# Kernel tuning notes

Measured on AMD Instinct MI355X. Metric: run time of the kernel, lower is better.

The kernel has to match this reference:

```python
import jax, jax.numpy as jnp
import numpy as np

B, T, C = 4, 1024, 1024
H, L = 16, 256
D = C // H  # head_dim = 64


def setup_inputs() -> dict:
    key = jax.random.key(0)
    ks = jax.random.split(key, 10)
    s = lambda fan_in: 1.0 / np.sqrt(fan_in)
    return {
        "x": jax.random.normal(ks[0], (B, T, C), jnp.float32),
        "padding_mask": jax.random.randint(ks[1], (B, T), 0, 2, jnp.int32),
        "interaction_matrix": jax.random.normal(ks[2], (B, T, T, H), jnp.float32),
        # weights stored [in, out] (x @ W == torch Linear with W = weight.T)
        "W_ckv": jax.random.uniform(ks[3], (C, L), jnp.float32, -s(C), s(C)),
        "W_cq": jax.random.uniform(ks[4], (C, L), jnp.float32, -s(C), s(C)),
        "W_kc": jax.random.uniform(ks[5], (L, C), jnp.float32, -s(L), s(L)),
        "W_qc": jax.random.uniform(ks[6], (L, C), jnp.float32, -s(L), s(L)),
        "W_vc": jax.random.uniform(ks[7], (L, C), jnp.float32, -s(L), s(L)),
        "W_proj": jax.random.uniform(ks[8], (C, C), jnp.float32, -s(C), s(C)),
        "b_proj": jax.random.uniform(ks[9], (C,), jnp.float32, -s(C), s(C)),
    }


def reference(x, padding_mask, interaction_matrix, W_ckv, W_cq, W_kc, W_qc, W_vc, W_proj, b_proj):
    # low-rank down/up projections
    kv_down = x @ W_ckv                      # [B,T,L]
    q_down = x @ W_cq                        # [B,T,L]
    k = (kv_down @ W_kc).reshape(B, T, H, D).transpose(0, 2, 1, 3)  # [B,H,T,D]
    q = (q_down @ W_qc).reshape(B, T, H, D).transpose(0, 2, 1, 3)
    v = (kv_down @ W_vc).reshape(B, T, H, D).transpose(0, 2, 1, 3)

    scores = jnp.einsum("bhqd,bhkd->bhqk", q, k) * (D ** -0.5)      # [B,H,T,T]

    # padding mask (fix=False path): mask[b,t]==0 masks query row t, fill -1e9
    row_mask = padding_mask[:, None, :, None]                        # [B,1,T,1]
    scores = jnp.where(row_mask == 0, jnp.float32(-1e9), scores)

    # causal mask
    causal = jnp.tril(jnp.ones((T, T), jnp.bool_))
    scores = jnp.where(causal, scores, -jnp.inf)

    # additive interaction bias: [B,T,T,H].transpose(1,3) -> [B,H,T,T]
    scores = scores + interaction_matrix.transpose(0, 3, 2, 1)

    attn = jax.nn.softmax(scores, axis=-1)                           # dropout=0 (eval)
    ctx = jnp.einsum("bhqk,bhkd->bhqd", attn, v)                     # [B,H,T,D]
    ctx = ctx.transpose(0, 2, 1, 3).reshape(B, T, C)
    return ctx @ W_proj + b_proj
```

## Files before the change

### kernel.cpp

```cpp
#include <hip/hip_runtime.h>

typedef unsigned short u16;
typedef unsigned int u32;
typedef __attribute__((ext_vector_type(8))) __bf16 bf16x8;
typedef __attribute__((ext_vector_type(4))) float f32x4;
typedef __attribute__((ext_vector_type(4))) short s16x4;
typedef __attribute__((ext_vector_type(4))) u32 u32x4;

#define LOG2E 1.4426950408889634f
#define NINF (-__builtin_inff())

static constexpr size_t OFF_WT_CKV = 0;
static constexpr size_t OFF_WT_CQ  = 262144;
static constexpr size_t OFF_WT_KC  = 524288;
static constexpr size_t OFF_WT_QC  = 786432;
static constexpr size_t OFF_WT_VC  = 1048576;
static constexpr size_t OFF_WT_PROJ= 1310720;
static constexpr size_t OFF_XBF    = 2359296;
static constexpr size_t OFF_DQ     = OFF_XBF + 4194304;
static constexpr size_t OFF_KB     = OFF_DQ  + 2097152;
static constexpr size_t OFF_QB     = OFF_KB  + 4194304;
static constexpr size_t OFF_VTB    = OFF_QB  + 4194304;
static constexpr size_t OFF_CTX    = OFF_XBF;

__device__ __forceinline__ u16 f2bf(float f) {
  u32 u = __builtin_bit_cast(u32, f);
  u = (u + 0x7fffu + ((u >> 16) & 1u)) >> 16;
  return (u16)u;
}

__device__ __forceinline__ void gld16(const void* g, void* l) {
  __builtin_amdgcn_global_load_lds(
      (const __attribute__((address_space(1))) u32*)(unsigned long long)g,
      (__attribute__((address_space(3))) u32*)(u32)(unsigned long long)l,
      16, 0, 0);
}

__global__ __launch_bounds__(256) void convert_kernel(
    const float* __restrict__ xin, const float* __restrict__ w0,
    const float* __restrict__ w1, const float* __restrict__ w2,
    const float* __restrict__ w3, const float* __restrict__ w4,
    const float* __restrict__ w5, u16* __restrict__ ws) {
  int gid = blockIdx.x * 256 + threadIdx.x;
  if (gid < 524288) {
    int i0 = gid * 8;
    f32x4 a = *(const f32x4*)(xin + i0);
    f32x4 b = *(const f32x4*)(xin + i0 + 4);
    u32x4 pv;
    pv[0] = (u32)f2bf(a[0]) | ((u32)f2bf(a[1]) << 16);
    pv[1] = (u32)f2bf(a[2]) | ((u32)f2bf(a[3]) << 16);
    pv[2] = (u32)f2bf(b[0]) | ((u32)f2bf(b[1]) << 16);
    pv[3] = (u32)f2bf(b[2]) | ((u32)f2bf(b[3]) << 16);
    *(u32x4*)(ws + OFF_XBF + i0) = pv;
    return;
  }
  int id = gid - 524288;
  if (id < 262144) { int k = id >> 8, n = id & 255;
    ws[OFF_WT_CKV + (size_t)n*1024 + k] = f2bf(w0[id]); return; }
  id -= 262144;
  if (id < 262144) { int k = id >> 8, n = id & 255;
    ws[OFF_WT_CQ + (size_t)n*1024 + k] = f2bf(w1[id]); return; }
  id -= 262144;
  if (id < 262144) { int k = id >> 10, n = id & 1023;
    ws[OFF_WT_KC + (size_t)n*256 + k] = f2bf(w2[id]); return; }
  id -= 262144;
  if (id < 262144) { int k = id >> 10, n = id & 1023;
    ws[OFF_WT_QC + (size_t)n*256 + k] = f2bf(w3[id]); return; }
  id -= 262144;
  if (id < 262144) { int k = id >> 10, n = id & 1023;
    ws[OFF_WT_VC + (size_t)n*256 + k] = f2bf(w4[id]); return; }
  id -= 262144;
  if (id < 1048576) { int k = id >> 10, n = id & 1023;
    ws[OFF_WT_PROJ + (size_t)n*1024 + k] = f2bf(w5[id]); return; }
}

template<int MODE, int MT, int NT>
__global__ __launch_bounds__(256, (MT == 128) ? 2 : 4) void gemm_kernel(
    const u16* __restrict__ A, const u16* __restrict__ BT,
    u16* __restrict__ ws, float* __restrict__ out, const float* __restrict__ bias) {
  constexpr int KDIM = (MODE == 1) ? 256 : 1024;
  constexpr int LDA  = (MODE == 1) ? 512 : 1024;
  constexpr int MW = MT / 32;
  constexpr int NW = NT / 32;
  __shared__ u16 lA[MT*32];
  __shared__ u16 lB[NT*32];
  const int t = threadIdx.x;
  const int lane = t & 63;
  const int c = lane & 15, quad = lane >> 4;
  const int w = t >> 6, wr = w >> 1, wc = w & 1;
  const int gm0 = blockIdx.y * MT, ct0 = blockIdx.x * NT;
  const u16* Ae = A;
  int out_id = 0;
  if (MODE == 1) { out_id = ct0 >> 10; if (out_id == 1) Ae += 256; }
  const int m0s = t >> 2, q0s = t & 3;

  f32x4 acc[MW][NW];
  #pragma unroll
  for (int i = 0; i < MW; ++i)
    #pragma unroll
    for (int j = 0; j < NW; ++j) acc[i][j] = (f32x4)0.0f;

  for (int k0 = 0; k0 < KDIM; k0 += 32) {
    __syncthreads();
    gld16(Ae + (size_t)(gm0 + m0s)*LDA + k0 + q0s*8, (char*)lA + t*16);
    if (MT == 128)
      gld16(Ae + (size_t)(gm0 + m0s + 64)*LDA + k0 + q0s*8, (char*)lA + (t+256)*16);
    gld16(BT + (size_t)(ct0 + m0s)*KDIM + k0 + q0s*8, (char*)lB + t*16);
    if (NT == 128)
      gld16(BT + (size_t)(ct0 + m0s + 64)*KDIM + k0 + q0s*8, (char*)lB + (t+256)*16);
    __syncthreads();
    bf16x8 af[MW], bfr[NW];
    #pragma unroll
    for (int mt = 0; mt < MW; ++mt)
      af[mt] = *(const bf16x8*)(lA + (wr*(MT/2) + mt*16 + c)*32 + quad*8);
    #pragma unroll
    for (int nt = 0; nt < NW; ++nt)
      bfr[nt] = *(const bf16x8*)(lB + (wc*(NT/2) + nt*16 + c)*32 + quad*8);
    #pragma unroll
    for (int mt = 0; mt < MW; ++mt)
      #pragma unroll
      for (int nt = 0; nt < NW; ++nt)
        acc[mt][nt] = __builtin_amdgcn_mfma_f32_16x16x32_bf16(af[mt], bfr[nt], acc[mt][nt], 0, 0, 0);
  }

  const int rbase = gm0 + wr*(MT/2);
  const int cbase = ct0 + wc*(NT/2);
  if (MODE == 0) {
    #pragma unroll
    for (int mt = 0; mt < MW; ++mt)
      #pragma unroll
      for (int nt = 0; nt < NW; ++nt)
        #pragma unroll
        for (int j = 0; j < 4; ++j) {
          int row = rbase + mt*16 + quad*4 + j;
          int col = cbase + nt*16 + c;
          ws[OFF_DQ + (size_t)row*512 + col] = f2bf(acc[mt][nt][j]);
        }
  } else if (MODE == 2) {
    float bv[NW];
    #pragma unroll
    for (int nt = 0; nt < NW; ++nt) bv[nt] = bias[cbase + nt*16 + c];
    #pragma unroll
    for (int mt = 0; mt < MW; ++mt)
      #pragma unroll
      for (int nt = 0; nt < NW; ++nt)
        #pragma unroll
        for (int j = 0; j < 4; ++j) {
          int row = rbase + mt*16 + quad*4 + j;
          out[(size_t)row*1024 + cbase + nt*16 + c] = acc[mt][nt][j] + bv[nt];
        }
  } else {
    const int cl = (ct0 & 1023) + wc*64;
    const int hcol = cl >> 6;
    if (out_id == 2) {
      #pragma unroll
      for (int mt = 0; mt < MW; ++mt) {
        int row0 = rbase + mt*16 + quad*4;
        int bb = row0 >> 10, t0 = row0 & 1023;
        #pragma unroll
        for (int nt = 0; nt < NW; ++nt) {
          int d = nt*16 + c;
          s16x4 pk;
          #pragma unroll
          for (int j = 0; j < 4; ++j) pk[j] = (short)f2bf(acc[mt][nt][j]);
          *(s16x4*)(ws + OFF_VTB + (((size_t)bb*16 + hcol)*64 + d)*1024 + t0) = pk;
        }
      }
    } else {
      const float sc = out_id ? 0.125f : 1.0f;
      const size_t base = out_id ? OFF_QB : OFF_KB;
      #pragma unroll
      for (int mt = 0; mt < MW; ++mt)
        #pragma unroll
        for (int nt = 0; nt < NW; ++nt)
          #pragma unroll
          for (int j = 0; j < 4; ++j) {
            int row = rbase + mt*16 + quad*4 + j;
            int bb = row >> 10, tt = row & 1023;
            ws[base + ((((size_t)bb*16 + hcol)*1024 + tt)<<6) + nt*16 + c]
                = f2bf(acc[mt][nt][j]*sc);
          }
    }
  }
}

__global__ __launch_bounds__(512, 2) void attn_kernel(
    const u16* __restrict__ Kb, const u16* __restrict__ Qb,
    const u16* __restrict__ VTb, u16* __restrict__ ctx,
    const float* __restrict__ im, const int* __restrict__ pmask) {
  __shared__ float lim[32*196];
  __shared__ u16   lp[8][16*40];

  const int t = threadIdx.x, lane = t & 63, w = t >> 6;
  const int c = lane & 15, quad = lane >> 4;
  const int bi = blockIdx.x;
  const int g = bi >> 4, hh = (bi >> 3) & 1, s = bi & 7;
  const int b = s >> 1, pair = g*2 + (s & 1);
  const int h0 = hh*8, h = h0 + w;
  const size_t bh = ((size_t)b*16 + h) << 16;

  const int k0s = t >> 5, q0s = (t & 31) >> 1, hp0 = (t & 1) * 4;
  const float* imb = im + ((size_t)b << 24) + h0;
  float* l0 = lim + k0s*196 + q0s*12 + hp0;
  float* l1 = lim + (k0s + 16)*196 + q0s*12 + hp0;

  const int qtA = 63 - pair;
  f32x4 r0 = *(const f32x4*)(imb + (((size_t)k0s)*1024 + qtA*16 + q0s)*16 + hp0);
  f32x4 r1 = *(const f32x4*)(imb + (((size_t)(k0s+16))*1024 + qtA*16 + q0s)*16 + hp0);

  for (int pass = 0; pass < 2; ++pass) {
    const int qt = pass ? pair : qtA;
    const int qrow0 = qt * 16;
    const int ktmax = (qrow0 + 15) >> 5;

    bf16x8 qf0 = *(const bf16x8*)(Qb + bh + (size_t)(qrow0 + c)*64 + quad*8);
    bf16x8 qf1 = *(const bf16x8*)(Qb + bh + (size_t)(qrow0 + c)*64 + 32 + quad*8);

    int tq[4], rm[4];
    #pragma unroll
    for (int j = 0; j < 4; ++j) {
      tq[j] = qrow0 + quad*4 + j;
      rm[j] = pmask[b*1024 + tq[j]];
    }
    float mr[4] = {NINF, NINF, NINF, NINF};
    float lr[4] = {0.f, 0.f, 0.f, 0.f};
    f32x4 O[4] = {(f32x4)0.f, (f32x4)0.f, (f32x4)0.f, (f32x4)0.f};

    for (int kt = 0; kt <= ktmax; ++kt) {
      const int kb = kt*32;
      __syncthreads();
      *(f32x4*)l0 = r0;
      *(f32x4*)l1 = r1;
      __syncthreads();
      if (kt < ktmax) {
        r0 = *(const f32x4*)(imb + (((size_t)(kb + 32 + k0s))*1024 + qrow0 + q0s)*16 + hp0);
        r1 = *(const f32x4*)(imb + (((size_t)(kb + 48 + k0s))*1024 + qrow0 + q0s)*16 + hp0);
      } else if (pass == 0) {
        r0 = *(const f32x4*)(imb + (((size_t)k0s)*1024 + pair*16 + q0s)*16 + hp0);
        r1 = *(const f32x4*)(imb + (((size_t)(k0s+16))*1024 + pair*16 + q0s)*16 + hp0);
      }

      f32x4 S[2] = {(f32x4)0.f, (f32x4)0.f};
      #pragma unroll
      for (int nt = 0; nt < 2; ++nt) {
        const u16* kp = Kb + bh + (size_t)(kb + nt*16 + c)*64 + quad*8;
        bf16x8 kf0 = *(const bf16x8*)kp;
        bf16x8 kf1 = *(const bf16x8*)(kp + 32);
        S[nt] = __builtin_amdgcn_mfma_f32_16x16x32_bf16(qf0, kf0, S[nt], 0, 0, 0);
        S[nt] = __builtin_amdgcn_mfma_f32_16x16x32_bf16(qf1, kf1, S[nt], 0, 0, 0);
      }
      #pragma unroll
      for (int nt = 0; nt < 2; ++nt) {
        int tk = kb + nt*16 + c;
        #pragma unroll
        for (int j = 0; j < 4; ++j) {
          float sv = S[nt][j] + lim[(nt*16 + c)*196 + (quad*4 + j)*12 + w];
          sv = rm[j] ? sv : 0.0f;
          sv = (tk <= tq[j]) ? sv : NINF;
          S[nt][j] = sv;
        }
      }
      float mn[4], al[4];
      #pragma unroll
      for (int j = 0; j < 4; ++j) {
        float vm = fmaxf(S[0][j], S[1][j]);
        vm = fmaxf(vm, __shfl_xor(vm, 1, 64));
        vm = fmaxf(vm, __shfl_xor(vm, 2, 64));
        vm = fmaxf(vm, __shfl_xor(vm, 4, 64));
        vm = fmaxf(vm, __shfl_xor(vm, 8, 64));
        mn[j] = fmaxf(mr[j], vm);
        al[j] = exp2f((mr[j] - mn[j]) * LOG2E);
        mr[j] = mn[j];
      }
      #pragma unroll
      for (int nt = 0; nt < 2; ++nt)
        #pragma unroll
        for (int j = 0; j < 4; ++j)
          S[nt][j] = exp2f((S[nt][j] - mn[j]) * LOG2E);
      #pragma unroll
      for (int j = 0; j < 4; ++j) {
        float sum = S[0][j] + S[1][j];
        sum += __shfl_xor(sum, 1, 64);
        sum += __shfl_xor(sum, 2, 64);
        sum += __shfl_xor(sum, 4, 64);
        sum += __shfl_xor(sum, 8, 64);
        lr[j] = lr[j]*al[j] + sum;
      }
      #pragma unroll
      for (int nd = 0; nd < 4; ++nd)
        #pragma unroll
        for (int j = 0; j < 4; ++j) O[nd][j] *= al[j];
      #pragma unroll
      for (int nt = 0; nt < 2; ++nt)
        #pragma unroll
        for (int j = 0; j < 4; ++j)
          lp[w][(quad*4 + j)*40 + nt*16 + c] = f2bf(S[nt][j]);
      bf16x8 pf = *(const bf16x8*)&lp[w][c*40 + quad*8];
      #pragma unroll
      for (int nd = 0; nd < 4; ++nd) {
        bf16x8 vf = *(const bf16x8*)(VTb + bh + (size_t)(nd*16 + c)*1024 + kb + quad*8);
        O[nd] = __builtin_amdgcn_mfma_f32_16x16x32_bf16(pf, vf, O[nd], 0, 0, 0);
      }
    }

    float inv[4];
    #pragma unroll
    for (int j = 0; j < 4; ++j) inv[j] = 1.0f / lr[j];
    #pragma unroll
    for (int nd = 0; nd < 4; ++nd)
      #pragma unroll
      for (int j = 0; j < 4; ++j)
        ctx[((size_t)b*1024 + tq[j])*1024 + h*64 + nd*16 + c] = f2bf(O[nd][j] * inv[j]);
  }
}

extern "C" void kernel_launch(void* const* d_in, const int* in_sizes, int n_in,
                              void* d_out, int out_size, void* d_ws, size_t ws_size,
                              hipStream_t stream) {
  const float* x     = (const float*)d_in[0];
  const int*   pm    = (const int*)d_in[1];
  const float* im    = (const float*)d_in[2];
  const float* wckv  = (const float*)d_in[3];
  const float* wcq   = (const float*)d_in[4];
  const float* wkc   = (const float*)d_in[5];
  const float* wqc   = (const float*)d_in[6];
  const float* wvc   = (const float*)d_in[7];
  const float* wproj = (const float*)d_in[8];
  const float* bproj = (const float*)d_in[9];
  u16* ws = (u16*)d_ws;
  float* out = (float*)d_out;

  convert_kernel<<<11264, 256, 0, stream>>>(x, wckv, wcq, wkc, wqc, wvc, wproj, ws);
  gemm_kernel<0,64,64><<<dim3(8, 64), 256, 0, stream>>>(ws + OFF_XBF, ws + OFF_WT_CKV, ws, nullptr, nullptr);
  gemm_kernel<1,128,128><<<dim3(24, 32), 256, 0, stream>>>(ws + OFF_DQ, ws + OFF_WT_KC, ws, nullptr, nullptr);
  attn_kernel<<<256, 512, 0, stream>>>(ws + OFF_KB, ws + OFF_QB, ws + OFF_VTB,
                                       ws + OFF_CTX, im, pm);
  gemm_kernel<2,64,128><<<dim3(8, 64), 256, 0, stream>>>(ws + OFF_CTX, ws + OFF_WT_PROJ, ws, out, bproj);
}
```

Baseline: 477.2 us.

## Software-pipeline attention loop with double-buffered bias and register K/V prefetch

Result: faster. 458.9 us (-3.8%).

```diff
diff --git a/kernel.cpp b/kernel.cpp
--- a/kernel.cpp
+++ b/kernel.cpp
@@ -34,6 +34,18 @@
       (const __attribute__((address_space(1))) u32*)(unsigned long long)g,
       (__attribute__((address_space(3))) u32*)(u32)(unsigned long long)l,
       16, 0, 0);
+}
+
+__device__ __forceinline__ void twrite(const float* __restrict__ w, u16* __restrict__ dst,
+                                       int n, int k0, int N, int R) {
+  u32x4 pv;
+  #pragma unroll
+  for (int jj = 0; jj < 4; ++jj) {
+    u32 lo = f2bf(w[(size_t)(k0 + 2*jj) * N + n]);
+    u32 hi = f2bf(w[(size_t)(k0 + 2*jj + 1) * N + n]);
+    pv[jj] = lo | (hi << 16);
+  }
+  *(u32x4*)(dst + (size_t)n * R + k0) = pv;
 }
 
 __global__ __launch_bounds__(256) void convert_kernel(
@@ -55,23 +67,23 @@
     return;
   }
   int id = gid - 524288;
-  if (id < 262144) { int k = id >> 8, n = id & 255;
-    ws[OFF_WT_CKV + (size_t)n*1024 + k] = f2bf(w0[id]); return; }
-  id -= 262144;
-  if (id < 262144) { int k = id >> 8, n = id & 255;
-    ws[OFF_WT_CQ + (size_t)n*1024 + k] = f2bf(w1[id]); return; }
-  id -= 262144;
-  if (id < 262144) { int k = id >> 10, n = id & 1023;
-    ws[OFF_WT_KC + (size_t)n*256 + k] = f2bf(w2[id]); return; }
-  id -= 262144;
-  if (id < 262144) { int k = id >> 10, n = id & 1023;
-    ws[OFF_WT_QC + (size_t)n*256 + k] = f2bf(w3[id]); return; }
-  id -= 262144;
-  if (id < 262144) { int k = id >> 10, n = id & 1023;
-    ws[OFF_WT_VC + (size_t)n*256 + k] = f2bf(w4[id]); return; }
-  id -= 262144;
-  if (id < 1048576) { int k = id >> 10, n = id & 1023;
-    ws[OFF_WT_PROJ + (size_t)n*1024 + k] = f2bf(w5[id]); return; }
+  if (id < 32768)  { int n = id >> 7, k0 = (id & 127) * 8;
+    twrite(w0, ws + OFF_WT_CKV, n, k0, 256, 1024); return; }
+  id -= 32768;
+  if (id < 32768)  { int n = id >> 7, k0 = (id & 127) * 8;
+    twrite(w1, ws + OFF_WT_CQ, n, k0, 256, 1024); return; }
+  id -= 32768;
+  if (id < 32768)  { int n = id >> 5, k0 = (id & 31) * 8;
+    twrite(w2, ws + OFF_WT_KC, n, k0, 1024, 256); return; }
+  id -= 32768;
+  if (id < 32768)  { int n = id >> 5, k0 = (id & 31) * 8;
+    twrite(w3, ws + OFF_WT_QC, n, k0, 1024, 256); return; }
+  id -= 32768;
+  if (id < 32768)  { int n = id >> 5, k0 = (id & 31) * 8;
+    twrite(w4, ws + OFF_WT_VC, n, k0, 1024, 256); return; }
+  id -= 32768;
+  if (id < 131072) { int n = id >> 7, k0 = (id & 127) * 8;
+    twrite(w5, ws + OFF_WT_PROJ, n, k0, 1024, 1024); return; }
 }
 
 template<int MODE, int MT, int NT>
@@ -188,7 +200,7 @@
     const u16* __restrict__ Kb, const u16* __restrict__ Qb,
     const u16* __restrict__ VTb, u16* __restrict__ ctx,
     const float* __restrict__ im, const int* __restrict__ pmask) {
-  __shared__ float lim[32*196];
+  __shared__ float lim[2][32*196];
   __shared__ u16   lp[8][16*40];
 
   const int t = threadIdx.x, lane = t & 63, w = t >> 6;
@@ -196,122 +208,163 @@
   const int bi = blockIdx.x;
   const int g = bi >> 4, hh = (bi >> 3) & 1, s = bi & 7;
   const int b = s >> 1, pair = g*2 + (s & 1);
-  const int h0 = hh*8, h = h0 + w;
+  const int h = hh*8 + w;
   const size_t bh = ((size_t)b*16 + h) << 16;
+  const int qtA = 63 - pair, qtB = pair;
+  const int ntA = ((qtA*16 + 15) >> 5) + 1;
 
   const int k0s = t >> 5, q0s = (t & 31) >> 1, hp0 = (t & 1) * 4;
-  const float* imb = im + ((size_t)b << 24) + h0;
-  float* l0 = lim + k0s*196 + q0s*12 + hp0;
-  float* l1 = lim + (k0s + 16)*196 + q0s*12 + hp0;
-
-  const int qtA = 63 - pair;
-  f32x4 r0 = *(const f32x4*)(imb + (((size_t)k0s)*1024 + qtA*16 + q0s)*16 + hp0);
-  f32x4 r1 = *(const f32x4*)(imb + (((size_t)(k0s+16))*1024 + qtA*16 + q0s)*16 + hp0);
-
-  for (int pass = 0; pass < 2; ++pass) {
-    const int qt = pass ? pair : qtA;
-    const int qrow0 = qt * 16;
-    const int ktmax = (qrow0 + 15) >> 5;
-
-    bf16x8 qf0 = *(const bf16x8*)(Qb + bh + (size_t)(qrow0 + c)*64 + quad*8);
-    bf16x8 qf1 = *(const bf16x8*)(Qb + bh + (size_t)(qrow0 + c)*64 + 32 + quad*8);
-
-    int tq[4], rm[4];
+  const float* imb = im + ((size_t)b << 24) + hh*8;
+  const int loff0 = k0s*196 + q0s*12 + hp0;
+  const int loff1 = (k0s + 16)*196 + q0s*12 + hp0;
+
+  int qrow = qtA * 16;
+  bf16x8 qf0 = *(const bf16x8*)(Qb + bh + (size_t)(qrow + c)*64 + quad*8);
+  bf16x8 qf1 = *(const bf16x8*)(Qb + bh + (size_t)(qrow + c)*64 + 32 + quad*8);
+  int tq[4], rm[4];
+  #pragma unroll
+  for (int j = 0; j < 4; ++j) {
+    tq[j] = qrow + quad*4 + j;
+    rm[j] = pmask[b*1024 + tq[j]];
+  }
+  float mr[4] = {NINF, NINF, NINF, NINF};
+  float lr[4] = {0.f, 0.f, 0.f, 0.f};
+  f32x4 O[4] = {(f32x4)0.f, (f32x4)0.f, (f32x4)0.f, (f32x4)0.f};
+
+  f32x4 r0 = *(const f32x4*)(imb + ((size_t)k0s*1024 + qrow + q0s)*16 + hp0);
+  f32x4 r1 = *(const f32x4*)(imb + ((size_t)(k0s+16)*1024 + qrow + q0s)*16 + hp0);
+  bf16x8 kc00 = *(const bf16x8*)(Kb + bh + (size_t)(c)*64 + quad*8);
+  bf16x8 kc01 = *(const bf16x8*)(Kb + bh + (size_t)(c)*64 + 32 + quad*8);
+  bf16x8 kc10 = *(const bf16x8*)(Kb + bh + (size_t)(16 + c)*64 + quad*8);
+  bf16x8 kc11 = *(const bf16x8*)(Kb + bh + (size_t)(16 + c)*64 + 32 + quad*8);
+  bf16x8 vc[4];
+  #pragma unroll
+  for (int nd = 0; nd < 4; ++nd)
+    vc[nd] = *(const bf16x8*)(VTb + bh + (size_t)(nd*16 + c)*1024 + quad*8);
+  *(f32x4*)(&lim[0][loff0]) = r0;
+  *(f32x4*)(&lim[0][loff1]) = r1;
+  __syncthreads();
+
+  for (int i = 0; i < 33; ++i) {
+    const int cb = i & 1;
+    const int kb = (i < ntA ? i : i - ntA) * 32;
+    const int ip = i + 1;
+    const bool havep = ip < 33;
+
+    bf16x8 kn00, kn01, kn10, kn11, vn[4];
+    if (havep) {
+      const int kbp = (ip < ntA ? ip : ip - ntA) * 32;
+      const int qrp = (ip < ntA ? qtA : qtB) * 16;
+      r0 = *(const f32x4*)(imb + ((size_t)(kbp + k0s)*1024 + qrp + q0s)*16 + hp0);
+      r1 = *(const f32x4*)(imb + ((size_t)(kbp + 16 + k0s)*1024 + qrp + q0s)*16 + hp0);
+      const u16* kp = Kb + bh + (size_t)(kbp + c)*64 + quad*8;
+      kn00 = *(const bf16x8*)kp;
+      kn01 = *(const bf16x8*)(kp + 32);
+      kn10 = *(const bf16x8*)(kp + 1024);
+      kn11 = *(const bf16x8*)(kp + 1056);
+      #pragma unroll
+      for (int nd = 0; nd < 4; ++nd)
+        vn[nd] = *(const bf16x8*)(VTb + bh + (size_t)(nd*16 + c)*1024 + kbp + quad*8);
+    }
+
+    f32x4 S[2] = {(f32x4)0.f, (f32x4)0.f};
+    S[0] = __builtin_amdgcn_mfma_f32_16x16x32_bf16(qf0, kc00, S[0], 0, 0, 0);
+    S[0] = __builtin_amdgcn_mfma_f32_16x16x32_bf16(qf1, kc01, S[0], 0, 0, 0);
+    S[1] = __builtin_amdgcn_mfma_f32_16x16x32_bf16(qf0, kc10, S[1], 0, 0, 0);
+    S[1] = __builtin_amdgcn_mfma_f32_16x16x32_bf16(qf1, kc11, S[1], 0, 0, 0);
+
+    #pragma unroll
+    for (int nt = 0; nt < 2; ++nt) {
+      int tk = kb + nt*16 + c;
+      #pragma unroll
+      for (int j = 0; j < 4; ++j) {
+        float sv = S[nt][j] + lim[cb][(nt*16 + c)*196 + (quad*4 + j)*12 + w];
+        sv = rm[j] ? sv : 0.0f;
+        sv = (tk <= tq[j]) ? sv : NINF;
+        S[nt][j] = sv;
+      }
+    }
+    float mn[4], al[4];
     #pragma unroll
     for (int j = 0; j < 4; ++j) {
-      tq[j] = qrow0 + quad*4 + j;
-      rm[j] = pmask[b*1024 + tq[j]];
-    }
-    float mr[4] = {NINF, NINF, NINF, NINF};
-    float lr[4] = {0.f, 0.f, 0.f, 0.f};
-    f32x4 O[4] = {(f32x4)0.f, (f32x4)0.f, (f32x4)0.f, (f32x4)0.f};
-
-    for (int kt = 0; kt <= ktmax; ++kt) {
-      const int kb = kt*32;
-      __syncthreads();
-      *(f32x4*)l0 = r0;
-      *(f32x4*)l1 = r1;
-      __syncthreads();
-      if (kt < ktmax) {
-        r0 = *(const f32x4*)(imb + (((size_t)(kb + 32 + k0s))*1024 + qrow0 + q0s)*16 + hp0);
-        r1 = *(const f32x4*)(imb + (((size_t)(kb + 48 + k0s))*1024 + qrow0 + q0s)*16 + hp0);
-      } else if (pass == 0) {
-        r0 = *(const f32x4*)(imb + (((size_t)k0s)*1024 + pair*16 + q0s)*16 + hp0);
-        r1 = *(const f32x4*)(imb + (((size_t)(k0s+16))*1024 + pair*16 + q0s)*16 + hp0);
+      float vm = fmaxf(S[0][j], S[1][j]);
+      vm = fmaxf(vm, __shfl_xor(vm, 1, 64));
+      vm = fmaxf(vm, __shfl_xor(vm, 2, 64));
+      vm = fmaxf(vm, __shfl_xor(vm, 4, 64));
+      vm = fmaxf(vm, __shfl_xor(vm, 8, 64));
+      mn[j] = fmaxf(mr[j], vm);
+      al[j] = exp2f((mr[j] - mn[j]) * LOG2E);
+      mr[j] = mn[j];
+    }
+    #pragma unroll
+    for (int nt = 0; nt < 2; ++nt)
+      #pragma unroll
+      for (int j = 0; j < 4; ++j)
+        S[nt][j] = exp2f((S[nt][j] - mn[j]) * LOG2E);
+    #pragma unroll
+    for (int j = 0; j < 4; ++j) {
+      float sum = S[0][j] + S[1][j];
+      sum += __shfl_xor(sum, 1, 64);
+      sum += __shfl_xor(sum, 2, 64);
+      sum += __shfl_xor(sum, 4, 64);
+      sum += __shfl_xor(sum, 8, 64);
+      lr[j] = lr[j]*al[j] + sum;
+    }
+    #pragma unroll
+    for (int nd = 0; nd < 4; ++nd)
+      #pragma unroll
+      for (int j = 0; j < 4; ++j) O[nd][j] *= al[j];
+    #pragma unroll
+    for (int nt = 0; nt < 2; ++nt)
+      #pragma unroll
+      for (int j = 0; j < 4; ++j)
+        lp[w][(quad*4 + j)*40 + nt*16 + c] = f2bf(S[nt][j]);
+    bf16x8 pf = *(const bf16x8*)&lp[w][c*40 + quad*8];
+    #pragma unroll
+    for (int nd = 0; nd < 4; ++nd)
+      O[nd] = __builtin_amdgcn_mfma_f32_16x16x32_bf16(pf, vc[nd], O[nd], 0, 0, 0);
+
+    if (havep) {
+      *(f32x4*)(&lim[cb ^ 1][loff0]) = r0;
+      *(f32x4*)(&lim[cb ^ 1][loff1]) = r1;
+    }
+    __syncthreads();
+    if (havep) {
+      kc00 = kn00; kc01 = kn01; kc10 = kn10; kc11 = kn11;
+      #pragma unroll
+      for (int nd = 0; nd < 4; ++nd) vc[nd] = vn[nd];
+    }
+
+    if (i == ntA - 1) {
+      float inv[4];
+      #pragma unroll
+      for (int j = 0; j < 4; ++j) inv[j] = 1.0f / lr[j];
+      #pragma unroll
+      for (int nd = 0; nd < 4; ++nd)
+        #pragma unroll
+        for (int j = 0; j < 4; ++j)
+          ctx[((size_t)b*1024 + tq[j])*1024 + h*64 + nd*16 + c] = f2bf(O[nd][j]*inv[j]);
+      qrow = qtB * 16;
+      qf0 = *(const bf16x8*)(Qb + bh + (size_t)(qrow + c)*64 + quad*8);
+      qf1 = *(const bf16x8*)(Qb + bh + (size_t)(qrow + c)*64 + 32 + quad*8);
+      #pragma unroll
+      for (int j = 0; j < 4; ++j) {
+        tq[j] = qrow + quad*4 + j;
+        rm[j] = pmask[b*1024 + tq[j]];
+        mr[j] = NINF; lr[j] = 0.f;
+        O[j] = (f32x4)0.f;
       }
-
-      f32x4 S[2] = {(f32x4)0.f, (f32x4)0.f};
-      #pragma unroll
-      for (int nt = 0; nt < 2; ++nt) {
-        const u16* kp = Kb + bh + (size_t)(kb + nt*16 + c)*64 + quad*8;
-        bf16x8 kf0 = *(const bf16x8*)kp;
-        bf16x8 kf1 = *(const bf16x8*)(kp + 32);
-        S[nt] = __builtin_amdgcn_mfma_f32_16x16x32_bf16(qf0, kf0, S[nt], 0, 0, 0);
-        S[nt] = __builtin_amdgcn_mfma_f32_16x16x32_bf16(qf1, kf1, S[nt], 0, 0, 0);
-      }
-      #pragma unroll
-      for (int nt = 0; nt < 2; ++nt) {
-        int tk = kb + nt*16 + c;
-        #pragma unroll
-        for (int j = 0; j < 4; ++j) {
-          float sv = S[nt][j] + lim[(nt*16 + c)*196 + (quad*4 + j)*12 + w];
-          sv = rm[j] ? sv : 0.0f;
-          sv = (tk <= tq[j]) ? sv : NINF;
-          S[nt][j] = sv;
-        }
-      }
-      float mn[4], al[4];
-      #pragma unroll
-      for (int j = 0; j < 4; ++j) {
-        float vm = fmaxf(S[0][j], S[1][j]);
-        vm = fmaxf(vm, __shfl_xor(vm, 1, 64));
-        vm = fmaxf(vm, __shfl_xor(vm, 2, 64));
-        vm = fmaxf(vm, __shfl_xor(vm, 4, 64));
-        vm = fmaxf(vm, __shfl_xor(vm, 8, 64));
-        mn[j] = fmaxf(mr[j], vm);
-        al[j] = exp2f((mr[j] - mn[j]) * LOG2E);
-        mr[j] = mn[j];
-      }
-      #pragma unroll
-      for (int nt = 0; nt < 2; ++nt)
-        #pragma unroll
-        for (int j = 0; j < 4; ++j)
-          S[nt][j] = exp2f((S[nt][j] - mn[j]) * LOG2E);
-      #pragma unroll
-      for (int j = 0; j < 4; ++j) {
-        float sum = S[0][j] + S[1][j];
-        sum += __shfl_xor(sum, 1, 64);
-        sum += __shfl_xor(sum, 2, 64);
-        sum += __shfl_xor(sum, 4, 64);
-        sum += __shfl_xor(sum, 8, 64);
-        lr[j] = lr[j]*al[j] + sum;
-      }
-      #pragma unroll
-      for (int nd = 0; nd < 4; ++nd)
-        #pragma unroll
-        for (int j = 0; j < 4; ++j) O[nd][j] *= al[j];
-      #pragma unroll
-      for (int nt = 0; nt < 2; ++nt)
-        #pragma unroll
-        for (int j = 0; j < 4; ++j)
-          lp[w][(quad*4 + j)*40 + nt*16 + c] = f2bf(S[nt][j]);
-      bf16x8 pf = *(const bf16x8*)&lp[w][c*40 + quad*8];
-      #pragma unroll
-      for (int nd = 0; nd < 4; ++nd) {
-        bf16x8 vf = *(const bf16x8*)(VTb + bh + (size_t)(nd*16 + c)*1024 + kb + quad*8);
-        O[nd] = __builtin_amdgcn_mfma_f32_16x16x32_bf16(pf, vf, O[nd], 0, 0, 0);
-      }
-    }
-
-    float inv[4];
-    #pragma unroll
-    for (int j = 0; j < 4; ++j) inv[j] = 1.0f / lr[j];
-    #pragma unroll
-    for (int nd = 0; nd < 4; ++nd)
-      #pragma unroll
-      for (int j = 0; j < 4; ++j)
-        ctx[((size_t)b*1024 + tq[j])*1024 + h*64 + nd*16 + c] = f2bf(O[nd][j] * inv[j]);
-  }
+    }
+  }
+
+  float inv[4];
+  #pragma unroll
+  for (int j = 0; j < 4; ++j) inv[j] = 1.0f / lr[j];
+  #pragma unroll
+  for (int nd = 0; nd < 4; ++nd)
+    #pragma unroll
+    for (int j = 0; j < 4; ++j)
+      ctx[((size_t)b*1024 + tq[j])*1024 + h*64 + nd*16 + c] = f2bf(O[nd][j]*inv[j]);
 }
 
 extern "C" void kernel_launch(void* const* d_in, const int* in_sizes, int n_in,
@@ -330,7 +383,7 @@
   u16* ws = (u16*)d_ws;
   float* out = (float*)d_out;
 
-  convert_kernel<<<11264, 256, 0, stream>>>(x, wckv, wcq, wkc, wqc, wvc, wproj, ws);
+  convert_kernel<<<3200, 256, 0, stream>>>(x, wckv, wcq, wkc, wqc, wvc, wproj, ws);
   gemm_kernel<0,64,64><<<dim3(8, 64), 256, 0, stream>>>(ws + OFF_XBF, ws + OFF_WT_CKV, ws, nullptr, nullptr);
   gemm_kernel<1,128,128><<<dim3(24, 32), 256, 0, stream>>>(ws + OFF_DQ, ws + OFF_WT_KC, ws, nullptr, nullptr);
   attn_kernel<<<256, 512, 0, stream>>>(ws + OFF_KB, ws + OFF_QB, ws + OFF_VTB,
```
